# Performance work log

Hardware: AMD Instinct MI355X
Metric: run time of the kernel (lower is better)

The kernel has to match this reference:

```python
import jax, jax.numpy as jnp
import numpy as np
from jax import lax

B_, L_, H_, P_ = 4, 8192, 1024, 64  # batch, seq, d_model, d_state//4
EPS = 1e-5


def setup_inputs() -> dict:
    key = jax.random.key(0)
    ks = jax.random.split(key, 20)
    s = 1.0 / np.sqrt(H_)
    inp = {
        "zH": jax.random.normal(ks[0], (B_, L_, H_), jnp.float32),
        "zL": jax.random.normal(ks[1], (B_, L_, H_), jnp.float32),
        "x": jax.random.normal(ks[2], (B_, L_, H_), jnp.float32),
        "t": jax.random.normal(ks[3], (B_, H_), jnp.float32),
        # AdaLN projections (d_model -> 2*d_model)
        "W_projH": jax.random.normal(ks[4], (H_, 2 * H_), jnp.float32) * s,
        "b_projH": jnp.zeros((2 * H_,), jnp.float32),
        "W_projL": jax.random.normal(ks[5], (H_, 2 * H_), jnp.float32) * s,
        "b_projL": jnp.zeros((2 * H_,), jnp.float32),
        # inj Linear (3*d_model -> d_model)
        "W_inj": jax.random.normal(ks[6], (3 * H_, H_), jnp.float32) * (1.0 / np.sqrt(3 * H_)),
        "b_inj": jnp.zeros((H_,), jnp.float32),
        # S5Dual params (diagonal complex SSM, bidirectional)
        "Lambda_re": -(0.1 + 0.4 * jax.random.uniform(ks[7], (P_,), jnp.float32)),
        "Lambda_im": jnp.pi * jnp.arange(P_, dtype=jnp.float32),
        "B_re": jax.random.normal(ks[8], (P_, H_), jnp.float32) * s,
        "B_im": jax.random.normal(ks[9], (P_, H_), jnp.float32) * s,
        "Cf_re": jax.random.normal(ks[10], (H_, P_), jnp.float32) * (1.0 / np.sqrt(P_)),
        "Cf_im": jax.random.normal(ks[11], (H_, P_), jnp.float32) * (1.0 / np.sqrt(P_)),
        "Cb_re": jax.random.normal(ks[12], (H_, P_), jnp.float32) * (1.0 / np.sqrt(P_)),
        "Cb_im": jax.random.normal(ks[13], (H_, P_), jnp.float32) * (1.0 / np.sqrt(P_)),
        "D": jax.random.normal(ks[14], (H_,), jnp.float32),
        "log_dt": jnp.log(0.001) + (jnp.log(0.1) - jnp.log(0.001)) * jax.random.uniform(ks[15], (P_,), jnp.float32),
    }
    return inp


def _adaln(x, cond, W, b):
    # x: [B,L,H], cond: [B,H]
    scale, shift = jnp.split(cond @ W + b, 2, axis=-1)
    mu = jnp.mean(x, axis=-1, keepdims=True)
    var = jnp.var(x, axis=-1, keepdims=True)
    xn = (x - mu) * lax.rsqrt(var + EPS)
    return xn * (1.0 + scale[:, None, :]) + shift[:, None, :]


def _binop(e1, e2):
    a1, b1 = e1
    a2, b2 = e2
    return a1 * a2, a2 * b1 + b2


def _s5_dual(u, Lambda_re, Lambda_im, B_re, B_im, Cf_re, Cf_im, Cb_re, Cb_im, D, log_dt):
    # u: [B,L,H] real -> [B,L,H] real. Bidirectional diagonal SSM (S5 style).
    Lam = Lambda_re + 1j * Lambda_im            # [P]
    dt = jnp.exp(log_dt)                        # [P]
    Lam_bar = jnp.exp(Lam * dt)                 # [P] ZOH discretization
    Bm = B_re + 1j * B_im                       # [P,H]
    B_bar = ((Lam_bar - 1.0) / Lam)[:, None] * Bm
    Bu = jnp.einsum('blh,ph->blp', u.astype(jnp.complex64), B_bar)  # [B,L,P]
    A = jnp.broadcast_to(Lam_bar, Bu.shape)
    xs_f = lax.associative_scan(_binop, (A, Bu), axis=1)[1]
    xs_b = jnp.flip(lax.associative_scan(_binop, (A, jnp.flip(Bu, axis=1)), axis=1)[1], axis=1)
    Cf = Cf_re + 1j * Cf_im
    Cb = Cb_re + 1j * Cb_im
    y = 2.0 * jnp.einsum('blp,hp->blh', xs_f, Cf).real \
        + 2.0 * jnp.einsum('blp,hp->blh', xs_b, Cb).real \
        + D * u
    return y


def reference(zH, zL, x, t, W_projH, b_projH, W_projL, b_projL, W_inj, b_inj,
              Lambda_re, Lambda_im, B_re, B_im, Cf_re, Cf_im, Cb_re, Cb_im, D, log_dt):
    zH = _adaln(zH, t, W_projH, b_projH)
    zL = _adaln(zL, t, W_projL, b_projL)
    h = jnp.concatenate([zH, zL, x], axis=-1)          # [B,L,3H]
    h = h @ W_inj + b_inj                              # [B,L,H]
    return _s5_dual(h, Lambda_re, Lambda_im, B_re, B_im, Cf_re, Cf_im, Cb_re, Cb_im, D, log_dt)
```

## Files before the change

### kernel.cpp

```cpp
#include <hip/hip_runtime.h>


#define LN_EPS 1e-5f

typedef __attribute__((ext_vector_type(8))) short bf16x8;
typedef __attribute__((ext_vector_type(8))) unsigned short u16x8;
typedef __attribute__((ext_vector_type(4))) float f32x4;

__device__ __forceinline__ unsigned short f2bf(float f) {
  unsigned int u = __float_as_uint(f);
  u += 0x7fffu + ((u >> 16) & 1u);
  return (unsigned short)(u >> 16);
}
__device__ __forceinline__ float bf2f(unsigned short s) {
  return __uint_as_float(((unsigned int)s) << 16);
}

__device__ __forceinline__ void gload16(const void* g, void* l) {
  __builtin_amdgcn_global_load_lds((const __attribute__((address_space(1))) void*)g,
                                   (__attribute__((address_space(3))) void*)l, 16, 0, 0);
}

__device__ __forceinline__ void phase_bar() {
  __builtin_amdgcn_sched_barrier(0);
  asm volatile("" ::: "memory");
  __builtin_amdgcn_s_barrier();
  __builtin_amdgcn_sched_barrier(0);
}

__global__ void proj_k(const float* __restrict__ t,
                       const float* __restrict__ WH, const float* __restrict__ bH,
                       const float* __restrict__ WL, const float* __restrict__ bL,
                       float* __restrict__ cond) {
  const int idx = blockIdx.x * 256 + threadIdx.x;
  const int tensor = idx >> 11;
  const int j2 = idx & 2047;
  const float* W = tensor ? WL : WH;
  const float bv = tensor ? bL[j2] : bH[j2];
  float a0 = bv, a1 = bv, a2 = bv, a3 = bv;
  #pragma unroll 4
  for (int k = 0; k < 1024; ++k) {
    const float w = W[k * 2048 + j2];
    a0 += t[k] * w; a1 += t[1024 + k] * w; a2 += t[2048 + k] * w; a3 += t[3072 + k] * w;
  }
  const int which = j2 >> 10, j = j2 & 1023;
  float* c = cond + (size_t)((tensor * 2 + which) * 4) * 1024 + j;
  c[0] = a0; c[1024] = a1; c[2048] = a2; c[3072] = a3;
}

__global__ void prep_k(const float* __restrict__ Winj, unsigned short* __restrict__ WinjT,
                       const float* __restrict__ Lre, const float* __restrict__ Lim,
                       const float* __restrict__ logdt,
                       const float* __restrict__ Bre, const float* __restrict__ Bim,
                       unsigned short* __restrict__ WBuT,
                       const float* __restrict__ t,
                       const float* __restrict__ WH, const float* __restrict__ WL,
                       float* __restrict__ part) {
  __shared__ float tl[64][65];
  const int bid = blockIdx.x;
  const int tid = threadIdx.x;
  if (bid < 768) {
    const int kt = bid >> 4, nt = bid & 15;
    const int k0 = kt << 6, n0 = nt << 6;
    #pragma unroll
    for (int s = 0; s < 4; ++s) {
      const int i = s * 256 + tid;
      const int r = i >> 4, c4 = i & 15;
      const float4 v = *(const float4*)&Winj[(size_t)(k0 + r) * 1024 + n0 + c4 * 4];
      tl[c4 * 4 + 0][r] = v.x; tl[c4 * 4 + 1][r] = v.y;
      tl[c4 * 4 + 2][r] = v.z; tl[c4 * 4 + 3][r] = v.w;
    }
    __syncthreads();
    const int i = tid >> 2, j0 = (tid & 3) << 4;
    u16x8 w0, w1;
    #pragma unroll
    for (int q = 0; q < 8; ++q) w0[q] = f2bf(tl[i][j0 + q]);
    #pragma unroll
    for (int q = 0; q < 8; ++q) w1[q] = f2bf(tl[i][j0 + 8 + q]);
    *(u16x8*)&WinjT[(size_t)(n0 + i) * 3072 + k0 + j0] = w0;
    *(u16x8*)&WinjT[(size_t)(n0 + i) * 3072 + k0 + j0 + 8] = w1;
  } else if (bid < 1280) {
    const int idx = (bid - 768) * 256 + tid;
    const int j = idx >> 10, hh = idx & 1023;
    const int p = j >> 1, im = j & 1;
    const float lr = Lre[p], li = Lim[p];
    const float dt = expf(logdt[p]);
    const float e = expf(lr * dt);
    float sn, cs; sincosf(li * dt, &sn, &cs);
    const float ar = e * cs - 1.f, ai = e * sn;
    const float den = lr * lr + li * li;
    const float cr = (ar * lr + ai * li) / den;
    const float ci = (ai * lr - ar * li) / den;
    const float br = Bre[p * 1024 + hh], bi = Bim[p * 1024 + hh];
    const float v = im ? (cr * bi + ci * br) : (cr * br - ci * bi);
    WBuT[idx] = f2bf(v);
  } else {
    const int pb = bid - 1280;
    const int tensor = pb >> 7, ks = (pb >> 3) & 15, jc = pb & 7;
    const int j2 = jc * 256 + tid;
    const float* W = tensor ? WL : WH;
    float a0 = 0.f, a1 = 0.f, a2 = 0.f, a3 = 0.f;
    const int k0 = ks * 64;
    #pragma unroll 4
    for (int k = k0; k < k0 + 64; ++k) {
      const float w = W[k * 2048 + j2];
      a0 += t[k] * w; a1 += t[1024 + k] * w; a2 += t[2048 + k] * w; a3 += t[3072 + k] * w;
    }
    float* p = part + ((size_t)(tensor * 16 + ks) * 4) * 2048 + j2;
    p[0] = a0; p[2048] = a1; p[4096] = a2; p[6144] = a3;
  }
}

__global__ void proj_red_k(const float* __restrict__ part,
                           const float* __restrict__ bH, const float* __restrict__ bL,
                           float* __restrict__ cond) {
  const int idx = blockIdx.x * 256 + threadIdx.x;
  const int tensor = idx >> 13, b = (idx >> 11) & 3, j2 = idx & 2047;
  float s = tensor ? bL[j2] : bH[j2];
  #pragma unroll
  for (int ks = 0; ks < 16; ++ks)
    s += part[((size_t)(tensor * 16 + ks) * 4 + b) * 2048 + j2];
  const int which = j2 >> 10, j = j2 & 1023;
  cond[((size_t)(tensor * 2 + which) * 4 + b) * 1024 + j] = s;
}

__global__ void transpose_winj(const float* __restrict__ W, unsigned short* __restrict__ WT) {
  __shared__ float tl[64][65];
  const int kt = blockIdx.x >> 4, nt = blockIdx.x & 15;
  const int k0 = kt << 6, n0 = nt << 6;
  const int tid = threadIdx.x;
  #pragma unroll
  for (int s = 0; s < 4; ++s) {
    const int i = s * 256 + tid;
    const int r = i >> 4, c4 = i & 15;
    const float4 v = *(const float4*)&W[(size_t)(k0 + r) * 1024 + n0 + c4 * 4];
    tl[c4 * 4 + 0][r] = v.x; tl[c4 * 4 + 1][r] = v.y;
    tl[c4 * 4 + 2][r] = v.z; tl[c4 * 4 + 3][r] = v.w;
  }
  __syncthreads();
  const int i = tid >> 2, j0 = (tid & 3) << 4;
  u16x8 w0, w1;
  #pragma unroll
  for (int q = 0; q < 8; ++q) w0[q] = f2bf(tl[i][j0 + q]);
  #pragma unroll
  for (int q = 0; q < 8; ++q) w1[q] = f2bf(tl[i][j0 + 8 + q]);
  *(u16x8*)&WT[(size_t)(n0 + i) * 3072 + k0 + j0] = w0;
  *(u16x8*)&WT[(size_t)(n0 + i) * 3072 + k0 + j0 + 8] = w1;
}

__global__ void wbu_k(const float* __restrict__ Lre, const float* __restrict__ Lim,
                      const float* __restrict__ logdt,
                      const float* __restrict__ Bre, const float* __restrict__ Bim,
                      unsigned short* __restrict__ WBuT) {
  const int idx = blockIdx.x * 256 + threadIdx.x;
  const int j = idx >> 10, hh = idx & 1023;
  const int p = j >> 1, im = j & 1;
  const float lr = Lre[p], li = Lim[p];
  const float dt = expf(logdt[p]);
  const float e = expf(lr * dt);
  float sn, cs; sincosf(li * dt, &sn, &cs);
  const float ar = e * cs - 1.f, ai = e * sn;
  const float den = lr * lr + li * li;
  const float cr = (ar * lr + ai * li) / den;
  const float ci = (ai * lr - ar * li) / den;
  const float br = Bre[p * 1024 + hh], bi = Bim[p * 1024 + hh];
  const float v = im ? (cr * bi + ci * br) : (cr * br - ci * bi);
  WBuT[idx] = f2bf(v);
}

__global__ void w2_k(const float* __restrict__ Cfre, const float* __restrict__ Cfim,
                     const float* __restrict__ Cbre, const float* __restrict__ Cbim,
                     unsigned short* __restrict__ W2T) {
  const int idx = blockIdx.x * 256 + threadIdx.x;
  const int h = idx >> 8, k = idx & 255;
  const int p = (k & 127) >> 1, im = k & 1, bw = k >> 7;
  const float* Cre = bw ? Cbre : Cfre;
  const float* Cim = bw ? Cbim : Cfim;
  const float v = im ? (-2.f * Cim[h * 64 + p]) : (2.f * Cre[h * 64 + p]);
  W2T[idx] = f2bf(v);
}

__global__ __launch_bounds__(256) void adaln_k(const float* __restrict__ zH,
                                               const float* __restrict__ zL,
                                               const float* __restrict__ x,
                                               const float* __restrict__ cond,
                                               unsigned short* __restrict__ znH,
                                               unsigned short* __restrict__ znL,
                                               unsigned short* __restrict__ xbf) {
  const int row = blockIdx.x;
  const int b = row >> 13;
  const int tid = threadIdx.x;
  const size_t rbase = (size_t)row * 1024;
  const float4 vH = *(const float4*)&zH[rbase + tid * 4];
  const float4 vL = *(const float4*)&zL[rbase + tid * 4];
  float sH = vH.x + vH.y + vH.z + vH.w;
  float qH = vH.x * vH.x + vH.y * vH.y + vH.z * vH.z + vH.w * vH.w;
  float sL = vL.x + vL.y + vL.z + vL.w;
  float qL = vL.x * vL.x + vL.y * vL.y + vL.z * vL.z + vL.w * vL.w;
  #pragma unroll
  for (int m = 1; m < 64; m <<= 1) {
    sH += __shfl_xor(sH, m); qH += __shfl_xor(qH, m);
    sL += __shfl_xor(sL, m); qL += __shfl_xor(qL, m);
  }
  __shared__ float red[4][4];
  const int wv = tid >> 6, ln = tid & 63;
  if (ln == 0) { red[wv][0] = sH; red[wv][1] = qH; red[wv][2] = sL; red[wv][3] = qL; }
  __syncthreads();
  sH = red[0][0] + red[1][0] + red[2][0] + red[3][0];
  qH = red[0][1] + red[1][1] + red[2][1] + red[3][1];
  sL = red[0][2] + red[1][2] + red[2][2] + red[3][2];
  qL = red[0][3] + red[1][3] + red[2][3] + red[3][3];
  const float muH = sH * (1.f / 1024.f);
  const float rsH = rsqrtf(qH * (1.f / 1024.f) - muH * muH + LN_EPS);
  const float muL = sL * (1.f / 1024.f);
  const float rsL = rsqrtf(qL * (1.f / 1024.f) - muL * muL + LN_EPS);
  const int h0 = tid * 4;
  const float4 scH = *(const float4*)&cond[(size_t)((0 * 2 + 0) * 4 + b) * 1024 + h0];
  const float4 shH = *(const float4*)&cond[(size_t)((0 * 2 + 1) * 4 + b) * 1024 + h0];
  const float4 scL = *(const float4*)&cond[(size_t)((1 * 2 + 0) * 4 + b) * 1024 + h0];
  const float4 shL = *(const float4*)&cond[(size_t)((1 * 2 + 1) * 4 + b) * 1024 + h0];
  ushort4 oH, oL;
  oH.x = f2bf((vH.x - muH) * rsH * (1.f + scH.x) + shH.x);
  oH.y = f2bf((vH.y - muH) * rsH * (1.f + scH.y) + shH.y);
  oH.z = f2bf((vH.z - muH) * rsH * (1.f + scH.z) + shH.z);
  oH.w = f2bf((vH.w - muH) * rsH * (1.f + scH.w) + shH.w);
  oL.x = f2bf((vL.x - muL) * rsL * (1.f + scL.x) + shL.x);
  oL.y = f2bf((vL.y - muL) * rsL * (1.f + scL.y) + shL.y);
  oL.z = f2bf((vL.z - muL) * rsL * (1.f + scL.z) + shL.z);
  oL.w = f2bf((vL.w - muL) * rsL * (1.f + scL.w) + shL.w);
  *(ushort4*)&znH[rbase + h0] = oH;
  *(ushort4*)&znL[rbase + h0] = oL;
  if (xbf != nullptr) {
    const float4 vx = *(const float4*)&x[rbase + h0];
    ushort4 ox;
    ox.x = f2bf(vx.x); ox.y = f2bf(vx.y); ox.z = f2bf(vx.z); ox.w = f2bf(vx.w);
    *(ushort4*)&xbf[rbase + h0] = ox;
  }
}

__global__ __launch_bounds__(512, 2) void gemm8p_k(
    const unsigned short* __restrict__ znH, const unsigned short* __restrict__ znL,
    const unsigned short* __restrict__ xbf, const unsigned short* __restrict__ WinjT,
    const float* __restrict__ binj, unsigned short* __restrict__ hout) {
  __shared__ char lds[131072];
  const int tid = threadIdx.x;
  const int ln = tid & 63;
  const int w = tid >> 6;
  const int wm = w >> 2, wn = w & 3;
  const int l15 = ln & 15, l4 = ln >> 4;
  const int swz = (blockIdx.x & 7) * 64 + (blockIdx.x >> 3);
  const int r0 = (swz >> 2) << 8, n0 = (swz & 3) << 8;
  constexpr int NT = 48;

  auto stageA = [&](int tau, int hf) {
    const int pidx = tau >> 4;
    const unsigned short* plane = pidx == 0 ? znH : (pidx == 1 ? znL : xbf);
    const int kbase = (tau & 15) << 6;
    char* dst0 = lds + (tau & 1) * 65536 + hf * 16384;
    #pragma unroll
    for (int i = 0; i < 2; ++i) {
      const int idx = i * 512 + tid;
      const int rl = idx >> 3, ps = idx & 7;
      const int ls = ps ^ (rl & 7);
      const unsigned short* src = plane + (size_t)(r0 + hf * 128 + rl) * 1024 + kbase + ls * 8;
      gload16(src, dst0 + i * 8192 + ((tid & 0x1C0) << 4));
    }
  };
  auto stageB = [&](int tau, int hf) {
    char* dst0 = lds + (tau & 1) * 65536 + 32768 + hf * 16384;
    #pragma unroll
    for (int i = 0; i < 2; ++i) {
      const int idx = i * 512 + tid;
      const int rl = idx >> 3, ps = idx & 7;
      const int ls = ps ^ (rl & 7);
      const unsigned short* src = WinjT + (size_t)(n0 + hf * 128 + rl) * 3072 + tau * 64 + ls * 8;
      gload16(src, dst0 + i * 8192 + ((tid & 0x1C0) << 4));
    }
  };
  auto ldA = [&](int tau, int m, int kk) -> bf16x8 {
    const int row = wm * 128 + m * 16 + l15;
    const int ps = (kk * 4 + l4) ^ (row & 7);
    return *(const bf16x8*)(lds + (tau & 1) * 65536 + row * 128 + ps * 16);
  };
  auto ldB = [&](int tau, int n, int kk) -> bf16x8 {
    const int row = wn * 64 + n * 16 + l15;
    const int ps = (kk * 4 + l4) ^ (row & 7);
    return *(const bf16x8*)(lds + (tau & 1) * 65536 + 32768 + row * 128 + ps * 16);
  };

  f32x4 acc[8][4];
  #pragma unroll
  for (int m = 0; m < 8; ++m)
    #pragma unroll
    for (int n = 0; n < 4; ++n)
      acc[m][n] = (f32x4){0.f, 0.f, 0.f, 0.f};

  stageA(0, 0); stageA(0, 1); stageB(0, 0); stageB(0, 1); stageA(1, 0); stageA(1, 1);
  asm volatile("s_waitcnt vmcnt(4)" ::: "memory");
  __builtin_amdgcn_s_barrier();
  __builtin_amdgcn_sched_barrier(0);

  for (int tau = 0; tau < NT; ++tau) {
    bf16x8 t0[4], c0[4], b0[4], t1[4], c1[4], b1[4];
    #pragma unroll
    for (int m = 0; m < 4; ++m) t0[m] = ldA(tau, m, 0);
    #pragma unroll
    for (int n = 0; n < 4; ++n) b0[n] = ldB(tau, n, 0);
    #pragma unroll
    for (int m = 0; m < 4; ++m) c0[m] = ldA(tau, m, 1);
    if (tau + 1 < NT) stageB(tau + 1, 0);
    phase_bar();
    __builtin_amdgcn_s_setprio(1);
    #pragma unroll
    for (int m = 0; m < 4; ++m)
      #pragma unroll
      for (int n = 0; n < 4; ++n)
        acc[m][n] = __builtin_amdgcn_mfma_f32_16x16x32_bf16(t0[m], b0[n], acc[m][n], 0, 0, 0);
    __builtin_amdgcn_s_setprio(0);
    phase_bar();
    #pragma unroll
    for (int m = 0; m < 4; ++m) t1[m] = ldA(tau, 4 + m, 0);
    #pragma unroll
    for (int m = 0; m < 4; ++m) c1[m] = ldA(tau, 4 + m, 1);
    if (tau + 1 < NT) stageB(tau + 1, 1);
    phase_bar();
    __builtin_amdgcn_s_setprio(1);
    #pragma unroll
    for (int m = 0; m < 4; ++m)
      #pragma unroll
      for (int n = 0; n < 4; ++n)
        acc[4 + m][n] = __builtin_amdgcn_mfma_f32_16x16x32_bf16(t1[m], b0[n], acc[4 + m][n], 0, 0, 0);
    __builtin_amdgcn_s_setprio(0);
    asm volatile("s_waitcnt lgkmcnt(0)" ::: "memory");
    phase_bar();
    #pragma unroll
    for (int n = 0; n < 4; ++n) b1[n] = ldB(tau, n, 1);
    if (tau + 2 < NT) stageA(tau + 2, 0);
    phase_bar();
    __builtin_amdgcn_s_setprio(1);
    #pragma unroll
    for (int m = 0; m < 4; ++m)
      #pragma unroll
      for (int n = 0; n < 4; ++n)
        acc[m][n] = __builtin_amdgcn_mfma_f32_16x16x32_bf16(c0[m], b1[n], acc[m][n], 0, 0, 0);
    __builtin_amdgcn_s_setprio(0);
    phase_bar();
    if (tau + 2 < NT) stageA(tau + 2, 1);
    if (tau < NT - 2) { asm volatile("s_waitcnt vmcnt(4)" ::: "memory"); }
    else              { asm volatile("s_waitcnt vmcnt(0)" ::: "memory"); }
    phase_bar();
    __builtin_amdgcn_s_setprio(1);
    #pragma unroll
    for (int m = 0; m < 4; ++m)
      #pragma unroll
      for (int n = 0; n < 4; ++n)
        acc[4 + m][n] = __builtin_amdgcn_mfma_f32_16x16x32_bf16(c1[m], b1[n], acc[4 + m][n], 0, 0, 0);
    __builtin_amdgcn_s_setprio(0);
    phase_bar();
  }

  #pragma unroll
  for (int n = 0; n < 4; ++n) {
    const int gcol = n0 + wn * 64 + n * 16 + l15;
    const float bv = binj[gcol];
    #pragma unroll
    for (int m = 0; m < 8; ++m) {
      const int grow = r0 + wm * 128 + m * 16 + l4 * 4;
      #pragma unroll
      for (int r = 0; r < 4; ++r)
        hout[(size_t)(grow + r) * 1024 + gcol] = f2bf(acc[m][n][r] + bv);
    }
  }
}

template<int KTOT, int NTOT, int CTILES, int EPI, int AMODE>
__global__ __launch_bounds__(256, 3) void gemm_k(
    const unsigned short* __restrict__ A,
    const unsigned short* __restrict__ Bm,
    const float* __restrict__ xsrc,
    const float* __restrict__ evec,
    const unsigned short* __restrict__ hbuf,
    void* __restrict__ Cout) {
  const int tid = threadIdx.x;
  const int wv = tid >> 6, ln = tid & 63;
  const int l15 = ln & 15, l4 = ln >> 4;
  const int wr = wv >> 1, wc = wv & 1;
  const int bid = blockIdx.x;
  const int rt = bid / CTILES, ct = bid % CTILES;
  const int r0 = rt << 7, n0 = ct << 7;

  __shared__ unsigned short ldsA[128 * 32];
  __shared__ unsigned short ldsB[128 * 32];

  f32x4 acc[4][4];
  #pragma unroll
  for (int i = 0; i < 4; ++i)
    #pragma unroll
    for (int j = 0; j < 4; ++j)
      acc[i][j] = (f32x4){0.f, 0.f, 0.f, 0.f};

  for (int k0 = 0; k0 < KTOT; k0 += 32) {
    __syncthreads();
    {
      const unsigned short* bb = Bm + (size_t)n0 * KTOT + k0;
      #pragma unroll
      for (int s0 = 0; s0 < 2; ++s0) {
        const int s = wv + s0 * 4;
        const int bo = (s << 10) + (ln << 4);
        const int row = bo >> 6, inb = bo & 63;
        gload16((const char*)(bb + (size_t)row * KTOT) + inb, (char*)ldsB + (s << 10));
      }
    }
    if (AMODE == 1 && k0 >= 2048) {
      const int row = tid >> 1, kf = (tid & 1) << 4;
      const float* xp = xsrc + (size_t)(r0 + row) * 1024 + (k0 - 2048) + kf;
      const float4 v0 = *(const float4*)(xp + 0);
      const float4 v1 = *(const float4*)(xp + 4);
      const float4 v2 = *(const float4*)(xp + 8);
      const float4 v3 = *(const float4*)(xp + 12);
      u16x8 w0, w1;
      w0[0] = f2bf(v0.x); w0[1] = f2bf(v0.y); w0[2] = f2bf(v0.z); w0[3] = f2bf(v0.w);
      w0[4] = f2bf(v1.x); w0[5] = f2bf(v1.y); w0[6] = f2bf(v1.z); w0[7] = f2bf(v1.w);
      w1[0] = f2bf(v2.x); w1[1] = f2bf(v2.y); w1[2] = f2bf(v2.z); w1[3] = f2bf(v2.w);
      w1[4] = f2bf(v3.x); w1[5] = f2bf(v3.y); w1[6] = f2bf(v3.z); w1[7] = f2bf(v3.w);
      *(u16x8*)&ldsA[row * 32 + kf] = w0;
      *(u16x8*)&ldsA[row * 32 + kf + 8] = w1;
    } else {
      const unsigned short* aa;
      int astr;
      if (AMODE == 0) { aa = A + (size_t)r0 * KTOT + k0; astr = KTOT; }
      else { aa = A + (size_t)(k0 >> 10) * (32768u * 1024u) + (size_t)r0 * 1024 + (k0 & 1023); astr = 1024; }
      #pragma unroll
      for (int s0 = 0; s0 < 2; ++s0) {
        const int s = wv + s0 * 4;
        const int bo = (s << 10) + (ln << 4);
        const int row = bo >> 6, inb = bo & 63;
        gload16((const char*)(aa + (size_t)row * astr) + inb, (char*)ldsA + (s << 10));
      }
    }
    __syncthreads();
    bf16x8 af[4], bfr[4];
    #pragma unroll
    for (int i = 0; i < 4; ++i)
      af[i] = *(const bf16x8*)&ldsA[(wr * 64 + i * 16 + l15) * 32 + l4 * 8];
    #pragma unroll
    for (int j = 0; j < 4; ++j)
      bfr[j] = *(const bf16x8*)&ldsB[(wc * 64 + j * 16 + l15) * 32 + l4 * 8];
    #pragma unroll
    for (int i = 0; i < 4; ++i)
      #pragma unroll
      for (int j = 0; j < 4; ++j)
        acc[i][j] = __builtin_amdgcn_mfma_f32_16x16x32_bf16(af[i], bfr[j], acc[i][j], 0, 0, 0);
  }

  #pragma unroll
  for (int j = 0; j < 4; ++j) {
    const int gcol = n0 + wc * 64 + j * 16 + l15;
    float ev = 0.f;
    if (EPI == 1 || EPI == 3) ev = evec[gcol];
    #pragma unroll
    for (int i = 0; i < 4; ++i) {
      const int gr = r0 + wr * 64 + i * 16 + l4 * 4;
      #pragma unroll
      for (int r = 0; r < 4; ++r) {
        const size_t idx = (size_t)(gr + r) * NTOT + gcol;
        const float v = acc[i][j][r];
        if (EPI == 1)      ((unsigned short*)Cout)[idx] = f2bf(v + ev);
        else if (EPI == 2) ((float*)Cout)[idx] = v;
        else               ((float*)Cout)[idx] = v + ev * bf2f(hbuf[idx]);
      }
    }
  }
}

__global__ void scan_agg_k(const float* __restrict__ Bu, float* __restrict__ agg,
                           const float* __restrict__ Lre, const float* __restrict__ Lim,
                           const float* __restrict__ logdt) {
  const int bid = blockIdx.x;
  const int dir = bid >> 8, b = (bid >> 6) & 3, ch = bid & 63;
  const int p = threadIdx.x;
  const float dt = expf(logdt[p]);
  const float e = expf(Lre[p] * dt);
  float sn, cs; sincosf(Lim[p] * dt, &sn, &cs);
  const float ar = e * cs, ai = e * sn;
  const int l0 = ch << 7;
  const float* base = Bu + ((size_t)b * 8192 + l0) * 128 + 2 * p;
  float sr = 0.f, si = 0.f;
  for (int g = 0; g < 16; ++g) {
    float2 v[8];
    #pragma unroll
    for (int u = 0; u < 8; ++u) {
      const int i = g * 8 + u;
      const int off = dir ? (127 - i) : i;
      v[u] = *(const float2*)(base + (size_t)off * 128);
    }
    #pragma unroll
    for (int u = 0; u < 8; ++u) {
      const float nr = ar * sr - ai * si + v[u].x;
      const float ni = ar * si + ai * sr + v[u].y;
      sr = nr; si = ni;
    }
  }
  float* o = agg + (((size_t)dir * 4 + b) * 64 + ch) * 128 + 2 * p;
  o[0] = sr; o[1] = si;
}

__global__ void scan_comb_k(const float* __restrict__ agg, float* __restrict__ pre,
                            const float* __restrict__ Lre, const float* __restrict__ Lim,
                            const float* __restrict__ logdt) {
  const int dir = blockIdx.x >> 2, b = blockIdx.x & 3;
  const int p = threadIdx.x;
  const float dt = expf(logdt[p]);
  const float e = expf(Lre[p] * dt);
  float sn, cs; sincosf(Lim[p] * dt, &sn, &cs);
  float Ar = e * cs, Ai = e * sn;
  #pragma unroll
  for (int q = 0; q < 7; ++q) {
    const float nr = Ar * Ar - Ai * Ai; Ai = 2.f * Ar * Ai; Ar = nr;
  }
  const float* ab = agg + ((size_t)(dir * 4 + b) * 64) * 128 + 2 * p;
  float* pb = pre + ((size_t)(dir * 4 + b) * 64) * 128 + 2 * p;
  float sr = 0.f, si = 0.f;
  for (int g = 0; g < 8; ++g) {
    float2 v[8];
    #pragma unroll
    for (int u = 0; u < 8; ++u) {
      const int i = g * 8 + u;
      const int ch = dir ? (63 - i) : i;
      v[u] = *(const float2*)(ab + (size_t)ch * 128);
    }
    #pragma unroll
    for (int u = 0; u < 8; ++u) {
      const int i = g * 8 + u;
      const int ch = dir ? (63 - i) : i;
      pb[(size_t)ch * 128] = sr; pb[(size_t)ch * 128 + 1] = si;
      const float nr = Ar * sr - Ai * si + v[u].x;
      const float ni = Ar * si + Ai * sr + v[u].y;
      sr = nr; si = ni;
    }
  }
}

__global__ void scan_apply_k(const float* __restrict__ Bu, const float* __restrict__ pre,
                             unsigned short* __restrict__ Xcat,
                             const float* __restrict__ Lre, const float* __restrict__ Lim,
                             const float* __restrict__ logdt) {
  const int bid = blockIdx.x;
  const int dir = bid >> 8, b = (bid >> 6) & 3, ch = bid & 63;
  const int p = threadIdx.x;
  const float dt = expf(logdt[p]);
  const float e = expf(Lre[p] * dt);
  float sn, cs; sincosf(Lim[p] * dt, &sn, &cs);
  const float ar = e * cs, ai = e * sn;
  const int l0 = ch << 7;
  const float* base = Bu + ((size_t)b * 8192 + l0) * 128 + 2 * p;
  const float* pr = pre + (((size_t)dir * 4 + b) * 64 + ch) * 128 + 2 * p;
  float sr = pr[0], si = pr[1];
  unsigned short* xb = Xcat + ((size_t)b * 8192 + l0) * 256 + dir * 128 + 2 * p;
  for (int g = 0; g < 16; ++g) {
    float2 v[8];
    #pragma unroll
    for (int u = 0; u < 8; ++u) {
      const int i = g * 8 + u;
      const int off = dir ? (127 - i) : i;
      v[u] = *(const float2*)(base + (size_t)off * 128);
    }
    #pragma unroll
    for (int u = 0; u < 8; ++u) {
      const int i = g * 8 + u;
      const int off = dir ? (127 - i) : i;
      const float nr = ar * sr - ai * si + v[u].x;
      const float ni = ar * si + ai * sr + v[u].y;
      sr = nr; si = ni;
      ushort2 ov; ov.x = f2bf(sr); ov.y = f2bf(si);
      *(ushort2*)(xb + (size_t)off * 256) = ov;
    }
  }
}

__global__ void scan_apply2_k(const float* __restrict__ Bu, const float* __restrict__ agg,
                              unsigned short* __restrict__ Xcat,
                              const float* __restrict__ Lre, const float* __restrict__ Lim,
                              const float* __restrict__ logdt) {
  const int bid = blockIdx.x;
  const int dir = bid >> 8, b = (bid >> 6) & 3, ch = bid & 63;
  const int p = threadIdx.x;
  const float dt = expf(logdt[p]);
  const float e = expf(Lre[p] * dt);
  float sn, cs; sincosf(Lim[p] * dt, &sn, &cs);
  const float ar = e * cs, ai = e * sn;
  float Ar = ar, Ai = ai;
  #pragma unroll
  for (int q = 0; q < 7; ++q) {
    const float nr = Ar * Ar - Ai * Ai; Ai = 2.f * Ar * Ai; Ar = nr;
  }
  const float* ab = agg + ((size_t)(dir * 4 + b) * 64) * 128 + 2 * p;
  float sr = 0.f, si = 0.f;
  const int nk = dir ? (63 - ch) : ch;
  for (int g0 = 0; g0 < nk; g0 += 8) {
    const int gn = (nk - g0) < 8 ? (nk - g0) : 8;
    float2 v[8];
    for (int u = 0; u < gn; ++u) {
      const int i = g0 + u;
      const int k = dir ? (63 - i) : i;
      v[u] = *(const float2*)(ab + (size_t)k * 128);
    }
    for (int u = 0; u < gn; ++u) {
      const float nr = Ar * sr - Ai * si + v[u].x;
      const float ni = Ar * si + Ai * sr + v[u].y;
      sr = nr; si = ni;
    }
  }
  const int l0 = ch << 7;
  const float* base = Bu + ((size_t)b * 8192 + l0) * 128 + 2 * p;
  unsigned short* xb = Xcat + ((size_t)b * 8192 + l0) * 256 + dir * 128 + 2 * p;
  for (int g = 0; g < 16; ++g) {
    float2 v[8];
    #pragma unroll
    for (int u = 0; u < 8; ++u) {
      const int i = g * 8 + u;
      const int off = dir ? (127 - i) : i;
      v[u] = *(const float2*)(base + (size_t)off * 128);
    }
    #pragma unroll
    for (int u = 0; u < 8; ++u) {
      const int i = g * 8 + u;
      const int off = dir ? (127 - i) : i;
      const float nr = ar * sr - ai * si + v[u].x;
      const float ni = ar * si + ai * sr + v[u].y;
      sr = nr; si = ni;
      ushort2 ov; ov.x = f2bf(sr); ov.y = f2bf(si);
      *(ushort2*)(xb + (size_t)off * 256) = ov;
    }
  }
}

extern "C" void kernel_launch(void* const* d_in, const int* in_sizes, int n_in,
                              void* d_out, int out_size, void* d_ws, size_t ws_size,
                              hipStream_t stream) {
  const float* zH    = (const float*)d_in[0];
  const float* zL    = (const float*)d_in[1];
  const float* x     = (const float*)d_in[2];
  const float* t     = (const float*)d_in[3];
  const float* WpH   = (const float*)d_in[4];
  const float* bpH   = (const float*)d_in[5];
  const float* WpL   = (const float*)d_in[6];
  const float* bpL   = (const float*)d_in[7];
  const float* Winj  = (const float*)d_in[8];
  const float* binj  = (const float*)d_in[9];
  const float* Lre   = (const float*)d_in[10];
  const float* Lim   = (const float*)d_in[11];
  const float* Bre   = (const float*)d_in[12];
  const float* Bim   = (const float*)d_in[13];
  const float* Cfre  = (const float*)d_in[14];
  const float* Cfim  = (const float*)d_in[15];
  const float* Cbre  = (const float*)d_in[16];
  const float* Cbim  = (const float*)d_in[17];
  const float* Dv    = (const float*)d_in[18];
  const float* logdt = (const float*)d_in[19];

  unsigned short* znH = (unsigned short*)d_out;
  unsigned short* znL = znH + (size_t)32768 * 1024;

  const bool FAST = ws_size >= 141950976ull;
  char* ws = (char*)d_ws;

  if (FAST) {
    unsigned short* WinjT = (unsigned short*)(ws + 0);
    unsigned short* hbuf  = (unsigned short*)(ws + 6291456);
    unsigned short* WBuT  = (unsigned short*)(ws + 73400320);
    float*          cond  = (float*)(ws + 73662464);
    float*          part  = (float*)(ws + 73793536);
    char*           U     = ws + 74842112;
    unsigned short* xbf   = (unsigned short*)U;
    float*          Bu    = (float*)(U + 0);
    float*          agg   = (float*)(U + 16777216);
    unsigned short* Xcat  = (unsigned short*)(U + 17301504);
    unsigned short* W2T   = (unsigned short*)(U + 34078720);

    prep_k<<<1536, 256, 0, stream>>>(Winj, WinjT, Lre, Lim, logdt, Bre, Bim, WBuT,
                                     t, WpH, WpL, part);
    proj_red_k<<<64, 256, 0, stream>>>(part, bpH, bpL, cond);
    adaln_k<<<32768, 256, 0, stream>>>(zH, zL, x, cond, znH, znL, xbf);
    gemm8p_k<<<512, 512, 0, stream>>>(znH, znL, xbf, WinjT, binj, hbuf);
    w2_k<<<1024, 256, 0, stream>>>(Cfre, Cfim, Cbre, Cbim, W2T);
    gemm_k<1024, 128, 1, 2, 0><<<256, 256, 0, stream>>>(hbuf, WBuT, nullptr, nullptr, nullptr, Bu);
    scan_agg_k<<<512, 64, 0, stream>>>(Bu, agg, Lre, Lim, logdt);
    scan_apply2_k<<<512, 64, 0, stream>>>(Bu, agg, Xcat, Lre, Lim, logdt);
    gemm_k<256, 1024, 8, 3, 0><<<2048, 256, 0, stream>>>(Xcat, W2T, nullptr, Dv, hbuf, (float*)d_out);
  } else {
    unsigned short* WinjT = (unsigned short*)ws; ws += (size_t)1024 * 3072 * 2;
    unsigned short* hbuf  = (unsigned short*)ws; ws += (size_t)32768 * 1024 * 2;
    unsigned short* WBuT  = (unsigned short*)ws; ws += (size_t)128 * 1024 * 2;
    float*          Bu    = (float*)ws;          ws += (size_t)32768 * 128 * 4;
    float*          cond  = (float*)ws;          ws += (size_t)2 * 2 * 4 * 1024 * 4;
    float*          agg   = (float*)ws;          ws += (size_t)2 * 4 * 64 * 128 * 4;
    float*          pre   = (float*)ws;          ws += (size_t)2 * 4 * 64 * 128 * 4;
    unsigned short* Xcat  = (unsigned short*)ws; ws += (size_t)32768 * 256 * 2;
    unsigned short* W2T   = (unsigned short*)ws; ws += (size_t)1024 * 256 * 2;

    proj_k<<<16, 256, 0, stream>>>(t, WpH, bpH, WpL, bpL, cond);
    transpose_winj<<<768, 256, 0, stream>>>(Winj, WinjT);
    wbu_k<<<512, 256, 0, stream>>>(Lre, Lim, logdt, Bre, Bim, WBuT);
    w2_k<<<1024, 256, 0, stream>>>(Cfre, Cfim, Cbre, Cbim, W2T);
    adaln_k<<<32768, 256, 0, stream>>>(zH, zL, x, cond, znH, znL, nullptr);
    gemm_k<3072, 1024, 8, 1, 1><<<2048, 256, 0, stream>>>(znH, WinjT, x, binj, nullptr, hbuf);
    gemm_k<1024, 128, 1, 2, 0><<<256, 256, 0, stream>>>(hbuf, WBuT, nullptr, nullptr, nullptr, Bu);
    scan_agg_k<<<512, 64, 0, stream>>>(Bu, agg, Lre, Lim, logdt);
    scan_comb_k<<<8, 64, 0, stream>>>(agg, pre, Lre, Lim, logdt);
    scan_apply_k<<<512, 64, 0, stream>>>(Bu, pre, Xcat, Lre, Lim, logdt);
    gemm_k<256, 1024, 8, 3, 0><<<2048, 256, 0, stream>>>(Xcat, W2T, nullptr, Dv, hbuf, (float*)d_out);
  }
}
```

Before: 452.0 us.

## Fuse Bu GEMM with chunk scan aggregation and W2 transpose into one kernel

Replaces three launches (w2_k, the Bu GEMM, scan_agg_k) with one gemm_bu_k kernel. Blocks past 256 build the W2T weight matrix, and the GEMM blocks stage their 128x128 output tile in LDS so two waves can compute the forward and backward chunk aggregates without re-reading Bu from global memory. This removes two launch overheads and one pass over Bu, but adds a 64KB LDS buffer that lowers occupancy and leaves a serial 128-step scan on two waves at the end of each GEMM block.

```diff
diff --git a/kernel.cpp b/kernel.cpp
--- a/kernel.cpp
+++ b/kernel.cpp
@@ -473,6 +473,113 @@
   }
 }
 
+__global__ __launch_bounds__(256) void gemm_bu_k(
+    const unsigned short* __restrict__ A, const unsigned short* __restrict__ Bm,
+    float* __restrict__ Bu, float* __restrict__ agg,
+    const float* __restrict__ Lre, const float* __restrict__ Lim,
+    const float* __restrict__ logdt,
+    const float* __restrict__ Cfre, const float* __restrict__ Cfim,
+    const float* __restrict__ Cbre, const float* __restrict__ Cbim,
+    unsigned short* __restrict__ W2T) {
+  const int tid = threadIdx.x;
+  if (blockIdx.x >= 256) {
+    const int idx = (blockIdx.x - 256) * 256 + tid;
+    const int h = idx >> 8, k = idx & 255;
+    const int p = (k & 127) >> 1, im = k & 1, bw = k >> 7;
+    const float* Cre = bw ? Cbre : Cfre;
+    const float* Cim = bw ? Cbim : Cfim;
+    const float v = im ? (-2.f * Cim[h * 64 + p]) : (2.f * Cre[h * 64 + p]);
+    W2T[idx] = f2bf(v);
+    return;
+  }
+  __shared__ unsigned short ldsA[128 * 32];
+  __shared__ unsigned short ldsB[128 * 32];
+  __shared__ float cbuf[128][128];
+  const int wv = tid >> 6, ln = tid & 63;
+  const int l15 = ln & 15, l4 = ln >> 4;
+  const int wr = wv >> 1, wc = wv & 1;
+  const int r0 = blockIdx.x << 7;
+
+  f32x4 acc[4][4];
+  #pragma unroll
+  for (int i = 0; i < 4; ++i)
+    #pragma unroll
+    for (int j = 0; j < 4; ++j)
+      acc[i][j] = (f32x4){0.f, 0.f, 0.f, 0.f};
+
+  for (int k0 = 0; k0 < 1024; k0 += 32) {
+    __syncthreads();
+    {
+      const unsigned short* bb = Bm + k0;
+      #pragma unroll
+      for (int s0 = 0; s0 < 2; ++s0) {
+        const int s = wv + s0 * 4;
+        const int bo = (s << 10) + (ln << 4);
+        const int row = bo >> 6, inb = bo & 63;
+        gload16((const char*)(bb + (size_t)row * 1024) + inb, (char*)ldsB + (s << 10));
+      }
+    }
+    {
+      const unsigned short* aa = A + (size_t)r0 * 1024 + k0;
+      #pragma unroll
+      for (int s0 = 0; s0 < 2; ++s0) {
+        const int s = wv + s0 * 4;
+        const int bo = (s << 10) + (ln << 4);
+        const int row = bo >> 6, inb = bo & 63;
+        gload16((const char*)(aa + (size_t)row * 1024) + inb, (char*)ldsA + (s << 10));
+      }
+    }
+    __syncthreads();
+    bf16x8 af[4], bfr[4];
+    #pragma unroll
+    for (int i = 0; i < 4; ++i)
+      af[i] = *(const bf16x8*)&ldsA[(wr * 64 + i * 16 + l15) * 32 + l4 * 8];
+    #pragma unroll
+    for (int j = 0; j < 4; ++j)
+      bfr[j] = *(const bf16x8*)&ldsB[(wc * 64 + j * 16 + l15) * 32 + l4 * 8];
+    #pragma unroll
+    for (int i = 0; i < 4; ++i)
+      #pragma unroll
+      for (int j = 0; j < 4; ++j)
+        acc[i][j] = __builtin_amdgcn_mfma_f32_16x16x32_bf16(af[i], bfr[j], acc[i][j], 0, 0, 0);
+  }
+
+  #pragma unroll
+  for (int j = 0; j < 4; ++j) {
+    const int lcol = wc * 64 + j * 16 + l15;
+    #pragma unroll
+    for (int i = 0; i < 4; ++i) {
+      const int lr0 = wr * 64 + i * 16 + l4 * 4;
+      #pragma unroll
+      for (int r = 0; r < 4; ++r) {
+        const float v = acc[i][j][r];
+        Bu[(size_t)(r0 + lr0 + r) * 128 + lcol] = v;
+        cbuf[lr0 + r][lcol] = v;
+      }
+    }
+  }
+  __syncthreads();
+  if (wv < 2) {
+    const int dir = wv, p = ln;
+    const float dt = expf(logdt[p]);
+    const float e = expf(Lre[p] * dt);
+    float sn, cs; sincosf(Lim[p] * dt, &sn, &cs);
+    const float ar = e * cs, ai = e * sn;
+    float sr = 0.f, si = 0.f;
+    for (int i = 0; i < 128; ++i) {
+      const int off = dir ? (127 - i) : i;
+      const float vr = cbuf[off][2 * p];
+      const float vi = cbuf[off][2 * p + 1];
+      const float nr = ar * sr - ai * si + vr;
+      const float ni = ar * si + ai * sr + vi;
+      sr = nr; si = ni;
+    }
+    const int b = r0 >> 13, ch = (r0 & 8191) >> 7;
+    float* o = agg + (((size_t)dir * 4 + b) * 64 + ch) * 128 + 2 * p;
+    o[0] = sr; o[1] = si;
+  }
+}
+
 __global__ void scan_agg_k(const float* __restrict__ Bu, float* __restrict__ agg,
                            const float* __restrict__ Lre, const float* __restrict__ Lim,
                            const float* __restrict__ logdt) {
@@ -683,9 +790,8 @@
     proj_red_k<<<64, 256, 0, stream>>>(part, bpH, bpL, cond);
     adaln_k<<<32768, 256, 0, stream>>>(zH, zL, x, cond, znH, znL, xbf);
     gemm8p_k<<<512, 512, 0, stream>>>(znH, znL, xbf, WinjT, binj, hbuf);
-    w2_k<<<1024, 256, 0, stream>>>(Cfre, Cfim, Cbre, Cbim, W2T);
-    gemm_k<1024, 128, 1, 2, 0><<<256, 256, 0, stream>>>(hbuf, WBuT, nullptr, nullptr, nullptr, Bu);
-    scan_agg_k<<<512, 64, 0, stream>>>(Bu, agg, Lre, Lim, logdt);
+    gemm_bu_k<<<1280, 256, 0, stream>>>(hbuf, WBuT, Bu, agg, Lre, Lim, logdt,
+                                        Cfre, Cfim, Cbre, Cbim, W2T);
     scan_apply2_k<<<512, 64, 0, stream>>>(Bu, agg, Xcat, Lre, Lim, logdt);
     gemm_k<256, 1024, 8, 3, 0><<<2048, 256, 0, stream>>>(Xcat, W2T, nullptr, Dv, hbuf, (float*)d_out);
   } else {
```

Result: no change. 449.7 us (-0.5%).
